# Kernel tuning notes

Hardware: AMD Instinct MI355X
Metric: run time of the kernel (lower is better)

## Reference

```python
import jax, jax.numpy as jnp
import numpy as np


def setup_inputs() -> dict:
    key = jax.random.key(0)
    ks = jax.random.split(key, 7)
    B, H, W = 32, 28, 28
    C3, C4 = 1024, 2048
    C = C3 + C4            # 3072
    L1 = 9                 # num_landmarks + 1
    A, NC = 312, 200
    return {
        "l3": jax.random.normal(ks[0], (B, C3, H, W), jnp.float32),
        "l4": jax.random.normal(ks[1], (B, C4, H // 2, W // 2), jnp.float32),
        "conv_w": jax.random.normal(ks[2], (L1, C), jnp.float32) * 0.02,
        "modulation": jnp.ones((1, C, L1), jnp.float32),
        "attr_w": jax.random.normal(ks[3], (A, C), jnp.float32) * 0.02,
        "attr_b": jnp.zeros((A,), jnp.float32),
        "class_w": jax.random.normal(ks[4], (NC, A), jnp.float32) * 0.02,
    }


def reference(l3, l4, conv_w, modulation, attr_w, attr_b, class_w):
    b, c3, h, w = l3.shape
    # F.interpolate(l4, (h, w), mode='bilinear', align_corners=False)
    l4_up = jax.image.resize(l4, (b, l4.shape[1], h, w), method="bilinear")
    x = jnp.concatenate([l4_up, l3], axis=1)            # (b, 3072, h, w)

    # 1x1 conv: ab[b,l,h,w] = sum_c w[l,c] * x[b,c,h,w]
    ab = jnp.einsum("lc,bchw->blhw", conv_w, x)
    b_sq = jnp.sum(x * x, axis=1, keepdims=True)        # (b,1,h,w)
    a_sq = jnp.sum(conv_w, axis=1)[None, :, None, None]  # (1,L+1,1,1)  (matches torch: weight.sum(1), NOT squared)
    maps = jax.nn.softmax(-(b_sq - 2.0 * ab + a_sq), axis=1)  # Softmax2d = softmax over channels

    # (maps[:,None] * x[:,:,None]).mean((-1,-2))  ->  batched GEMM over spatial dim
    all_features = jnp.einsum("blhw,bchw->bcl", maps, x) / (h * w)  # (b, c, L+1)

    mod = all_features * modulation                     # dropout is identity at eval
    # permute(0,2,1)[:, :-1, :].mean(1) == mean over landmark dim excluding background
    mean_features = jnp.mean(mod[:, :, :-1], axis=2)    # (b, c)

    attr_scores = mean_features @ attr_w.T + attr_b      # (b, 312)
    class_scores = attr_scores @ class_w.T               # (b, 200)
    return attr_scores, class_scores, maps, all_features
```

## Files before the change

kernel.cpp:

```cpp
#include <hip/hip_runtime.h>
#include <math.h>

#define B_    32
#define C3_   1024
#define C4_   2048
#define C_    3072
#define P_    784
#define Q_    196
#define L_    9
#define NG_   25088
#define A_    312
#define NC_   200

#define ATTR_OFF  0
#define CLASS_OFF 9984
#define MAPS_OFF  16384
#define AF_OFF    242176

#define ASQ_OFF   0
#define MF_OFF    16
#define PART3_OFF 98320
#define PAF_OFF   98320
#define Y4P_OFF   (PART3_OFF + 16 * 9 * NG_)
#define LOGITS_OFF Y4P_OFF
#define Y_OFF     (Y4P_OFF + 32 * 32 * 9 * Q_)
#define MP_OFF    (Y_OFF + 32 * 9 * Q_)

typedef __attribute__((ext_vector_type(8))) short bf16x8;
typedef __attribute__((ext_vector_type(4))) float f32x4;

__device__ __forceinline__ short f2bf(float f) {
    union { float f; unsigned u; } v; v.f = f;
    unsigned r = v.u + 0x7FFFu + ((v.u >> 16) & 1u);
    return (short)(r >> 16);
}

__global__ __launch_bounds__(256, 2) void kA(
        const float* __restrict__ l3, const float* __restrict__ l4,
        const float* __restrict__ conv_w,
        float* __restrict__ part3, float* __restrict__ y4p) {
    int bid = blockIdx.x;
    int t = threadIdx.x;

    const float* xp;
    float* outp;
    int xpitch, opitch, cbase_w;
    if (bid < 784) {
        int slab = bid / 49, rb = bid % 49;
        int tid2 = rb * 256 + t;
        int b = tid2 / 392, px = (tid2 % 392) * 2;
        xp = l3 + ((size_t)b * C3_ + slab * 64) * P_ + px;
        xpitch = P_;
        cbase_w = C4_ + slab * 64;
        outp = part3 + (size_t)(slab * 9) * NG_ + b * P_ + px;
        opitch = NG_;
    } else {
        int idx = bid - 784;
        int grp = idx / 13, rb = idx % 13;
        int tid2 = rb * 256 + t;
        if (tid2 >= 3136) return;
        int b = tid2 / 98, q = (tid2 % 98) * 2;
        xp = l4 + ((size_t)b * C4_ + grp * 64) * Q_ + q;
        xpitch = Q_;
        cbase_w = grp * 64;
        outp = y4p + ((size_t)(b * 32 + grp) * 9) * Q_ + q;
        opitch = Q_;
    }

    float acc[9][2];
#pragma unroll
    for (int l = 0; l < 9; ++l) {
        acc[l][0] = 0.f; acc[l][1] = 0.f;
    }

    float2 v[2][8];
#pragma unroll
    for (int k = 0; k < 8; ++k)
        v[0][k] = *(const float2*)(xp + (size_t)k * xpitch);

#pragma unroll
    for (int c = 0; c < 64; c += 8) {
        int cur = (c >> 3) & 1, nxt = cur ^ 1;
        if (c < 56) {
#pragma unroll
            for (int k = 0; k < 8; ++k)
                v[nxt][k] = *(const float2*)(xp + (size_t)(c + 8 + k) * xpitch);
        }
#pragma unroll
        for (int l = 0; l < 9; ++l) {
            const float4 w0 = *(const float4*)(conv_w + l * C_ + cbase_w + c);
            const float4 w1 = *(const float4*)(conv_w + l * C_ + cbase_w + c + 4);
            const float wv[8] = {w0.x, w0.y, w0.z, w0.w, w1.x, w1.y, w1.z, w1.w};
#pragma unroll
            for (int k = 0; k < 8; ++k) {
                acc[l][0] = fmaf(wv[k], v[cur][k].x, acc[l][0]);
                acc[l][1] = fmaf(wv[k], v[cur][k].y, acc[l][1]);
            }
        }
    }
#pragma unroll
    for (int l = 0; l < 9; ++l)
        *(float2*)(outp + (size_t)l * opitch) = make_float2(acc[l][0], acc[l][1]);
}

__global__ __launch_bounds__(256) void kB(const float* __restrict__ y4p,
                                          const float* __restrict__ conv_w,
                                          float* __restrict__ Y,
                                          float* __restrict__ asq) {
    if (blockIdx.x == 221) {
        __shared__ float red[256];
        int t = threadIdx.x;
        for (int l = 0; l < L_; ++l) {
            float s = 0.f;
            for (int c = t; c < C_; c += 256) s += conv_w[l * C_ + c];
            red[t] = s; __syncthreads();
            for (int o = 128; o > 0; o >>= 1) {
                if (t < o) red[t] += red[t + o];
                __syncthreads();
            }
            if (t == 0) asq[l] = red[0];
            __syncthreads();
        }
        return;
    }
    int tid = blockIdx.x * 256 + threadIdx.x;
    if (tid >= 32 * 9 * Q_) return;
    int b = tid / (9 * Q_);
    int r = tid % (9 * Q_);
    float s = 0.f;
#pragma unroll
    for (int grp = 0; grp < 32; ++grp)
        s += y4p[(size_t)(b * 32 + grp) * (9 * Q_) + r];
    Y[(size_t)b * (9 * Q_) + r] = s;
}

__global__ __launch_bounds__(256) void kC1(const float* __restrict__ part3,
                                           const float* __restrict__ Y,
                                           const float* __restrict__ asq,
                                           float* __restrict__ logits) {
    int idx = blockIdx.x * 256 + threadIdx.x;
    int l = idx / NG_, g = idx % NG_;
    int b = g / P_, p = g % P_;
    int yy = p / 28, xx = p % 28;
    float sy = 0.5f * yy - 0.25f, sx = 0.5f * xx - 0.25f;
    float fyf = floorf(sy), fxf = floorf(sx);
    float fy = sy - fyf, fx = sx - fxf;
    int ya = max(0, (int)fyf), yb = min(13, (int)fyf + 1);
    int xa = max(0, (int)fxf), xb = min(13, (int)fxf + 1);
    float w00 = (1.f - fy) * (1.f - fx), w01 = (1.f - fy) * fx;
    float w10 = fy * (1.f - fx),         w11 = fy * fx;
    const float* Yl = Y + ((size_t)b * 9 + l) * Q_;
    float ab4 = w00 * Yl[ya * 14 + xa] + w01 * Yl[ya * 14 + xb]
              + w10 * Yl[yb * 14 + xa] + w11 * Yl[yb * 14 + xb];
    float ab3 = 0.f;
#pragma unroll
    for (int sl = 0; sl < 16; ++sl)
        ab3 += part3[(size_t)(sl * 9 + l) * NG_ + g];
    logits[idx] = 2.f * (ab4 + ab3) - asq[l];
}

__global__ __launch_bounds__(256) void kC2(const float* __restrict__ logits,
                                           float* __restrict__ out_maps) {
    int g = blockIdx.x * 256 + threadIdx.x;
    int b = g / P_, p = g % P_;
    float v[9];
#pragma unroll
    for (int l = 0; l < 9; ++l) v[l] = logits[(size_t)l * NG_ + g];
    float m = v[0];
#pragma unroll
    for (int l = 1; l < 9; ++l) m = fmaxf(m, v[l]);
    float sum = 0.f;
#pragma unroll
    for (int l = 0; l < 9; ++l) { v[l] = expf(v[l] - m); sum += v[l]; }
    float inv = 1.f / sum;
#pragma unroll
    for (int l = 0; l < 9; ++l)
        out_maps[(size_t)b * (L_ * P_) + l * P_ + p] = v[l] * inv;
}

__device__ __forceinline__ int adj_taps(int q, int* ys, float* wy) {
    if (q == 0)  { ys[0] = 0;  wy[0] = 1.00f; ys[1] = 1;  wy[1] = 0.75f;
                   ys[2] = 2;  wy[2] = 0.25f; return 3; }
    if (q == 13) { ys[0] = 25; wy[0] = 0.25f; ys[1] = 26; wy[1] = 0.75f;
                   ys[2] = 27; wy[2] = 1.00f; return 3; }
    ys[0] = 2 * q - 1; wy[0] = 0.25f;
    ys[1] = 2 * q;     wy[1] = 0.75f;
    ys[2] = 2 * q + 1; wy[2] = 0.75f;
    ys[3] = 2 * q + 2; wy[3] = 0.25f;
    return 4;
}

__global__ __launch_bounds__(256) void kD(const float* __restrict__ maps,
                                          float* __restrict__ Mp) {
    int tid = blockIdx.x * 256 + threadIdx.x;
    if (tid >= 32 * 9 * Q_) return;
    int b = tid / (9 * Q_);
    int r = tid % (9 * Q_);
    int l = r / Q_, q = r % Q_;
    int qy = q / 14, qx = q % 14;
    int ys[4], xs[4]; float wy[4], wx[4];
    int ny = adj_taps(qy, ys, wy);
    int nx = adj_taps(qx, xs, wx);
    const float* mrow = maps + (size_t)b * (L_ * P_) + l * P_;
    float s = 0.f;
    for (int i = 0; i < ny; ++i) {
        float rs = 0.f;
        for (int j = 0; j < nx; ++j)
            rs = fmaf(wx[j], mrow[ys[i] * 28 + xs[j]], rs);
        s = fmaf(wy[i], rs, s);
    }
    Mp[(size_t)b * (9 * Q_) + r] = s;
}

#define SA 232
__global__ __launch_bounds__(256) void kE(
        const float* __restrict__ l3, const float* __restrict__ l4,
        const float* __restrict__ maps, const float* __restrict__ Mp,
        float* __restrict__ out_af, float* __restrict__ paf) {
    __shared__ short As[64 * SA];
    __shared__ short Bs[16 * SA];
    int bid = blockIdx.x;
    int t = threadIdx.x;
    int wave = t >> 6, lane = t & 63;
    int row16 = lane & 15, quad = lane >> 4;

    const float* xsrc; size_t xstride;
    const float* bsrc; size_t bstride;
    int b, c0, h;
    bool isl4 = (bid < 1024);
    if (isl4) {
        b = bid >> 5;
        c0 = (bid & 31) * 64;
        h = 0;
        xsrc = l4 + ((size_t)b * C4_ + c0) * Q_;
        xstride = Q_;
        bsrc = Mp + (size_t)b * (9 * Q_);
        bstride = Q_;
    } else {
        int idx = bid - 1024;
        b = idx >> 6;
        c0 = ((idx >> 2) & 15) * 64;
        h = idx & 3;
        xsrc = l3 + ((size_t)b * C3_ + c0) * P_ + h * Q_;
        xstride = P_;
        bsrc = maps + (size_t)b * (L_ * P_) + h * Q_;
        bstride = P_;
    }

    for (int i = t; i < 64 * 49; i += 256) {
        int r = i / 49, j = (i % 49) * 4;
        float4 v = *(const float4*)(xsrc + (size_t)r * xstride + j);
        ushort4 o;
        o.x = (unsigned short)f2bf(v.x); o.y = (unsigned short)f2bf(v.y);
        o.z = (unsigned short)f2bf(v.z); o.w = (unsigned short)f2bf(v.w);
        *(ushort4*)(As + r * SA + j) = o;
    }
    for (int i = t; i < 64 * 9; i += 256) {
        int r = i / 9, j = 196 + (i % 9) * 4;
        *(ushort4*)(As + r * SA + j) = make_ushort4(0, 0, 0, 0);
    }
    for (int i = t; i < 16 * 58; i += 256) {
        int r = i / 58, j = (i % 58) * 4;
        ushort4 o = make_ushort4(0, 0, 0, 0);
        if (r < 9 && j < 196) {
            float4 v = *(const float4*)(bsrc + (size_t)r * bstride + j);
            o.x = (unsigned short)f2bf(v.x); o.y = (unsigned short)f2bf(v.y);
            o.z = (unsigned short)f2bf(v.z); o.w = (unsigned short)f2bf(v.w);
        }
        *(ushort4*)(Bs + r * SA + j) = o;
    }
    __syncthreads();

    const short* arow = As + (wave * 16 + row16) * SA;
    const short* brow = Bs + row16 * SA;
    f32x4 acc = {0.f, 0.f, 0.f, 0.f};
#pragma unroll
    for (int k0 = 0; k0 < 224; k0 += 32) {
        bf16x8 a = *(const bf16x8*)(arow + k0 + quad * 8);
        bf16x8 bv = *(const bf16x8*)(brow + k0 + quad * 8);
        acc = __builtin_amdgcn_mfma_f32_16x16x32_bf16(a, bv, acc, 0, 0, 0);
    }
    int l = row16;
    if (l < 9) {
        int c = c0 + wave * 16 + quad * 4;
        if (isl4) {
            size_t base = ((size_t)b * C_ + c) * 9 + l;
#pragma unroll
            for (int r = 0; r < 4; ++r)
                out_af[base + (size_t)r * 9] = acc[r] * (1.f / 784.f);
        } else {
            size_t base = ((size_t)(h * B_ + b) * C3_ + c) * 9 + l;
#pragma unroll
            for (int r = 0; r < 4; ++r)
                paf[base + (size_t)r * 9] = acc[r];
        }
    }
}

__global__ __launch_bounds__(256) void kMF(const float* __restrict__ paf,
                                           const float* __restrict__ mod,
                                           float* __restrict__ out_af,
                                           float* __restrict__ mf) {
    int i = blockIdx.x * 256 + threadIdx.x;
    if (i >= B_ * C_) return;
    int b = i / C_, c = i % C_;
    float af[9];
    if (c < C4_) {
#pragma unroll
        for (int l = 0; l < 9; ++l) af[l] = out_af[(size_t)i * 9 + l];
    } else {
        int c3 = c - C4_;
#pragma unroll
        for (int l = 0; l < 9; ++l) {
            float s = 0.f;
#pragma unroll
            for (int hh = 0; hh < 4; ++hh)
                s += paf[((size_t)(hh * B_ + b) * C3_ + c3) * 9 + l];
            af[l] = s * (1.f / 784.f);
            out_af[(size_t)i * 9 + l] = af[l];
        }
    }
    const float* m = mod + (size_t)c * 9;
    float s = 0.f;
#pragma unroll
    for (int l = 0; l < 8; ++l) s = fmaf(af[l], m[l], s);
    mf[i] = s * 0.125f;
}

__global__ __launch_bounds__(256) void kF(
        const float* __restrict__ mf, const float* __restrict__ attr_w,
        const float* __restrict__ attr_b, float* __restrict__ out_attr) {
    int idx = blockIdx.x * 4 + (threadIdx.x >> 6);
    int lane = threadIdx.x & 63;
    int b = idx / A_, a = idx % A_;
    const float4* wr = (const float4*)(attr_w + (size_t)a * C_);
    const float4* mr = (const float4*)(mf + (size_t)b * C_);
    float acc = 0.f;
    for (int j = lane; j < C_ / 4; j += 64) {
        float4 w = wr[j], m = mr[j];
        acc += w.x * m.x + w.y * m.y + w.z * m.z + w.w * m.w;
    }
    acc += __shfl_xor(acc, 1);  acc += __shfl_xor(acc, 2);
    acc += __shfl_xor(acc, 4);  acc += __shfl_xor(acc, 8);
    acc += __shfl_xor(acc, 16); acc += __shfl_xor(acc, 32);
    if (lane == 0) out_attr[idx] = acc + attr_b[a];
}

__global__ __launch_bounds__(256) void kG(
        const float* __restrict__ attr, const float* __restrict__ class_w,
        float* __restrict__ out_class) {
    int idx = blockIdx.x * 4 + (threadIdx.x >> 6);
    int lane = threadIdx.x & 63;
    int b = idx / NC_, n = idx % NC_;
    float acc = 0.f;
    for (int a = lane; a < A_; a += 64)
        acc += attr[b * A_ + a] * class_w[n * A_ + a];
    acc += __shfl_xor(acc, 1);  acc += __shfl_xor(acc, 2);
    acc += __shfl_xor(acc, 4);  acc += __shfl_xor(acc, 8);
    acc += __shfl_xor(acc, 16); acc += __shfl_xor(acc, 32);
    if (lane == 0) out_class[idx] = acc;
}

extern "C" void kernel_launch(void* const* d_in, const int* in_sizes, int n_in,
                              void* d_out, int out_size, void* d_ws, size_t ws_size,
                              hipStream_t stream) {
    (void)in_sizes; (void)n_in; (void)out_size; (void)ws_size;
    const float* l3         = (const float*)d_in[0];
    const float* l4         = (const float*)d_in[1];
    const float* conv_w     = (const float*)d_in[2];
    const float* modulation = (const float*)d_in[3];
    const float* attr_w     = (const float*)d_in[4];
    const float* attr_b     = (const float*)d_in[5];
    const float* class_w    = (const float*)d_in[6];
    float* out = (float*)d_out;
    float* ws  = (float*)d_ws;
    float* asq    = ws + ASQ_OFF;
    float* mf     = ws + MF_OFF;
    float* part3  = ws + PART3_OFF;
    float* paf    = ws + PAF_OFF;
    float* y4p    = ws + Y4P_OFF;
    float* logits = ws + LOGITS_OFF;
    float* Y      = ws + Y_OFF;
    float* Mp     = ws + MP_OFF;

    kA<<<1200, 256, 0, stream>>>(l3, l4, conv_w, part3, y4p);
    kB<<<222, 256, 0, stream>>>(y4p, conv_w, Y, asq);
    kC1<<<882, 256, 0, stream>>>(part3, Y, asq, logits);
    kC2<<<98, 256, 0, stream>>>(logits, out + MAPS_OFF);
    kD<<<221, 256, 0, stream>>>(out + MAPS_OFF, Mp);
    kE<<<3072, 256, 0, stream>>>(l3, l4, out + MAPS_OFF, Mp, out + AF_OFF, paf);
    kMF<<<384, 256, 0, stream>>>(paf, modulation, out + AF_OFF, mf);
    kF<<<(B_ * A_) / 4, 256, 0, stream>>>(mf, attr_w, attr_b, out + ATTR_OFF);
    kG<<<(B_ * NC_) / 4, 256, 0, stream>>>(out + ATTR_OFF, class_w,
                                           out + CLASS_OFF);
}
```

Before: 304.1 us.

## Stage kA input tiles into LDS with direct global-to-LDS loads

Result: slower. 347.6 us (+14.3%).

```diff
diff --git a/kernel.cpp b/kernel.cpp
--- a/kernel.cpp
+++ b/kernel.cpp
@@ -35,72 +35,72 @@
     return (short)(r >> 16);
 }
 
+#define GLDS16(gp, lp) __builtin_amdgcn_global_load_lds(                    \
+        (const __attribute__((address_space(1))) unsigned int*)(gp),        \
+        (__attribute__((address_space(3))) unsigned int*)(lp), 16, 0, 0)
+
 __global__ __launch_bounds__(256, 2) void kA(
         const float* __restrict__ l3, const float* __restrict__ l4,
         const float* __restrict__ conv_w,
         float* __restrict__ part3, float* __restrict__ y4p) {
+    __shared__ float X[64 * 256];
     int bid = blockIdx.x;
     int t = threadIdx.x;
-
-    const float* xp;
-    float* outp;
-    int xpitch, opitch, cbase_w;
-    if (bid < 784) {
-        int slab = bid / 49, rb = bid % 49;
-        int tid2 = rb * 256 + t;
-        int b = tid2 / 392, px = (tid2 % 392) * 2;
-        xp = l3 + ((size_t)b * C3_ + slab * 64) * P_ + px;
-        xpitch = P_;
+    int wave = t >> 6, lane = t & 63;
+
+    bool isl3 = (bid < 1568);
+    int slab = 0, g0 = 0, b = 0, grp = 0, cbase_w;
+    const float* gbase;
+    size_t rowpitch;
+    if (isl3) {
+        slab = bid / 98;
+        g0 = (bid % 98) * 256;
+        int gidx = g0 + lane * 4;
+        int bb = gidx / 784, px = gidx % 784;
+        gbase = l3 + ((size_t)bb * C3_ + slab * 64) * P_ + px;
+        rowpitch = P_;
         cbase_w = C4_ + slab * 64;
-        outp = part3 + (size_t)(slab * 9) * NG_ + b * P_ + px;
-        opitch = NG_;
     } else {
-        int idx = bid - 784;
-        int grp = idx / 13, rb = idx % 13;
-        int tid2 = rb * 256 + t;
-        if (tid2 >= 3136) return;
-        int b = tid2 / 98, q = (tid2 % 98) * 2;
-        xp = l4 + ((size_t)b * C4_ + grp * 64) * Q_ + q;
-        xpitch = Q_;
+        int idx = bid - 1568;
+        b = idx >> 5; grp = idx & 31;
+        int q = lane * 4;
+        if (q > 192) q = 192;
+        gbase = l4 + ((size_t)b * C4_ + grp * 64) * Q_ + q;
+        rowpitch = Q_;
         cbase_w = grp * 64;
-        outp = y4p + ((size_t)(b * 32 + grp) * 9) * Q_ + q;
-        opitch = Q_;
-    }
-
-    float acc[9][2];
-#pragma unroll
-    for (int l = 0; l < 9; ++l) {
-        acc[l][0] = 0.f; acc[l][1] = 0.f;
-    }
-
-    float2 v[2][8];
-#pragma unroll
-    for (int k = 0; k < 8; ++k)
-        v[0][k] = *(const float2*)(xp + (size_t)k * xpitch);
-
-#pragma unroll
-    for (int c = 0; c < 64; c += 8) {
-        int cur = (c >> 3) & 1, nxt = cur ^ 1;
-        if (c < 56) {
-#pragma unroll
-            for (int k = 0; k < 8; ++k)
-                v[nxt][k] = *(const float2*)(xp + (size_t)(c + 8 + k) * xpitch);
-        }
-#pragma unroll
-        for (int l = 0; l < 9; ++l) {
-            const float4 w0 = *(const float4*)(conv_w + l * C_ + cbase_w + c);
-            const float4 w1 = *(const float4*)(conv_w + l * C_ + cbase_w + c + 4);
-            const float wv[8] = {w0.x, w0.y, w0.z, w0.w, w1.x, w1.y, w1.z, w1.w};
-#pragma unroll
-            for (int k = 0; k < 8; ++k) {
-                acc[l][0] = fmaf(wv[k], v[cur][k].x, acc[l][0]);
-                acc[l][1] = fmaf(wv[k], v[cur][k].y, acc[l][1]);
-            }
-        }
-    }
-#pragma unroll
-    for (int l = 0; l < 9; ++l)
-        *(float2*)(outp + (size_t)l * opitch) = make_float2(acc[l][0], acc[l][1]);
+    }
+
+#pragma unroll
+    for (int k = 0; k < 16; ++k) {
+        int row = k * 4 + wave;
+        GLDS16(gbase + (size_t)row * rowpitch, &X[row * 256]);
+    }
+    asm volatile("s_waitcnt vmcnt(0)" ::: "memory");
+    __builtin_amdgcn_s_barrier();
+    asm volatile("" ::: "memory");
+
+    float acc[9];
+#pragma unroll
+    for (int l = 0; l < 9; ++l) acc[l] = 0.f;
+
+    if (isl3 || t < 196) {
+#pragma unroll
+        for (int c = 0; c < 64; ++c) {
+            float x = X[c * 256 + t];
+#pragma unroll
+            for (int l = 0; l < 9; ++l)
+                acc[l] = fmaf(conv_w[(size_t)l * C_ + cbase_w + c], x, acc[l]);
+        }
+        if (isl3) {
+            float* op = part3 + (size_t)(slab * 9) * NG_ + g0 + t;
+#pragma unroll
+            for (int l = 0; l < 9; ++l) op[(size_t)l * NG_] = acc[l];
+        } else {
+            float* op = y4p + ((size_t)(b * 32 + grp) * 9) * Q_ + t;
+#pragma unroll
+            for (int l = 0; l < 9; ++l) op[l * Q_] = acc[l];
+        }
+    }
 }
 
 __global__ __launch_bounds__(256) void kB(const float* __restrict__ y4p,
@@ -383,7 +383,7 @@
     float* Y      = ws + Y_OFF;
     float* Mp     = ws + MP_OFF;
 
-    kA<<<1200, 256, 0, stream>>>(l3, l4, conv_w, part3, y4p);
+    kA<<<2592, 256, 0, stream>>>(l3, l4, conv_w, part3, y4p);
     kB<<<222, 256, 0, stream>>>(y4p, conv_w, Y, asq);
     kC1<<<882, 256, 0, stream>>>(part3, Y, asq, logits);
     kC2<<<98, 256, 0, stream>>>(logits, out + MAPS_OFF);
```
